# Kernel optimization log

Hardware: AMD Instinct MI355X
Metric: run time of the kernel (lower is better)

## Reference

```python
import jax, jax.numpy as jnp
import numpy as np

# Static graph layout: B equal-sized graphs of N nodes, DEG random edges per node.
B, N, DEG = 128, 1024, 16
F_IN, H, C = 2, 64, 2
RATIO = 0.8
E = B * N * DEG
K1 = int(np.ceil(RATIO * N))      # 820
K2 = int(np.ceil(RATIO * K1))     # 656
K3 = int(np.ceil(RATIO * K2))     # 525


def setup_inputs() -> dict:
    key = jax.random.key(0)
    ks = jax.random.split(key, 24)
    x = jax.random.normal(ks[0], (B * N, F_IN), jnp.float32)
    edge_attr = jax.random.uniform(ks[1], (E,), jnp.float32)
    # per-graph random endpoints, offset so edges stay inside each graph
    local = jax.random.randint(ks[2], (2, B, N * DEG), 0, N)
    edge_index = (local + (jnp.arange(B) * N)[None, :, None]).reshape(2, E)

    def lin(k, i, o):
        return jax.random.normal(k, (i, o), jnp.float32) / np.sqrt(i)

    def bias(k, o):
        return jax.random.normal(k, (o,), jnp.float32) * 0.01

    return {
        "x": x, "edge_attr": edge_attr,
        "W1": lin(ks[3], F_IN, H), "b1": bias(ks[4], H),
        "Wp1": lin(ks[5], H, 1), "bp1": bias(ks[6], 1),
        "W2": lin(ks[7], H, H), "b2": bias(ks[8], H),
        "Wp2": lin(ks[9], H, 1), "bp2": bias(ks[10], 1),
        "W3": lin(ks[11], H, H), "b3": bias(ks[12], H),
        "Wp3": lin(ks[13], H, 1), "bp3": bias(ks[14], 1),
        "Wl1": lin(ks[15], 2 * H, H), "bl1": bias(ks[16], H),
        "Wl2": lin(ks[17], H, H // 2), "bl2": bias(ks[18], H // 2),
        "Wl3": lin(ks[19], H // 2, C), "bl3": bias(ks[20], C),
        "edge_index": edge_index,
    }


def gcn(x, src, dst, w, W, b):
    """PyG GCNConv with gcn_norm (self-loops weight 1)."""
    h = x @ W                                       # [BN, out]
    deg = jnp.zeros((x.shape[0],), x.dtype).at[dst].add(w) + 1.0
    dinv = jax.lax.rsqrt(deg)
    norm = dinv[src] * w * dinv[dst]                # [E]
    out = jnp.zeros_like(h).at[dst].add(norm[:, None] * h[src])
    out = out + (dinv * dinv)[:, None] * h          # self-loop term
    return out + b


def sagpool(x, alive, src, dst, Wp, bp, k):
    """SAGPool: unweighted GCN scoring, per-graph top-k, x <- x * tanh(score).
    Removed nodes/edges are kept as masked (alive=False) slots -> static shapes."""
    we = (alive[src] & alive[dst]).astype(x.dtype)
    score = gcn(x, src, dst, we, Wp, bp)[:, 0]      # [BN]
    s = jnp.where(alive, score, -jnp.inf).reshape(B, N)
    _, idx = jax.lax.top_k(s, k)                    # [B, k]
    alive_new = jnp.zeros((B, N), bool).at[jnp.arange(B)[:, None], idx].set(True).reshape(-1)
    xn = jnp.where(alive_new[:, None], x * jnp.tanh(score)[:, None], 0.0)
    return xn, alive_new


def readout(x, alive):
    """concat(global_max_pool, global_mean_pool) over alive nodes per graph."""
    xr = x.reshape(B, N, -1)
    m = alive.reshape(B, N, 1)
    mx = jnp.max(jnp.where(m, xr, -jnp.inf), axis=1)
    mn = jnp.sum(jnp.where(m, xr, 0.0), axis=1) / jnp.sum(m, axis=1).astype(x.dtype)
    return jnp.concatenate([mx, mn], axis=1)        # [B, 2*H]


def _forward(x, edge_attr, W1, b1, Wp1, bp1, W2, b2, Wp2, bp2, W3, b3, Wp3, bp3,
             Wl1, bl1, Wl2, bl2, Wl3, bl3, edge_index):
    src, dst = edge_index[0], edge_index[1]
    h = jax.nn.relu(gcn(x, src, dst, edge_attr, W1, b1))
    h, a1 = sagpool(h, jnp.ones((B * N,), bool), src, dst, Wp1, bp1, K1)
    x1 = readout(h, a1)

    ea1 = edge_attr * (a1[src] & a1[dst]).astype(x.dtype)
    h = jax.nn.relu(gcn(h, src, dst, ea1, W2, b2))
    h, a2 = sagpool(h, a1, src, dst, Wp2, bp2, K2)
    x2 = readout(h, a2)

    # conv3 is called WITHOUT edge_weight -> surviving edges get weight 1
    ea2 = (a2[src] & a2[dst]).astype(x.dtype)
    h = jax.nn.relu(gcn(h, src, dst, ea2, W3, b3))
    h, a3 = sagpool(h, a2, src, dst, Wp3, bp3, K3)
    x3 = readout(h, a3)

    g = x1 + x2 + x3
    g = jax.nn.relu(g @ Wl1 + bl1)                  # dropout: eval mode (identity)
    g = jax.nn.relu(g @ Wl2 + bl2)
    return jax.nn.log_softmax(g @ Wl3 + bl3, axis=-1)


def reference(x, edge_attr, W1, b1, Wp1, bp1, W2, b2, Wp2, bp2, W3, b3, Wp3, bp3,
              Wl1, bl1, Wl2, bl2, Wl3, bl3, edge_index):
    return _forward(x, edge_attr, W1, b1, Wp1, bp1, W2, b2, Wp2, bp2, W3, b3,
                    Wp3, bp3, Wl1, bl1, Wl2, bl2, Wl3, bl3, edge_index)
```

## Files before the change

kernel.cpp:

```cpp
#include <hip/hip_runtime.h>
#include <math.h>

#define NB 128
#define NN 1024
#define BNODES (NB*NN)
#define NE 2097152
#define EPG (NE/NB)
#define EPT (EPG/NN)
#define FH 64
#define KK1 820
#define KK2 656
#define KK3 525

__global__ __launch_bounds__(1024) void k_csr(const int* __restrict__ ei,
                                              const float* __restrict__ ea,
                                              int* __restrict__ rowptr,
                                              int2* __restrict__ csr_sw,
                                              int* __restrict__ aliveA,
                                              float* __restrict__ dinvW,
                                              float* __restrict__ dinvU) {
  extern __shared__ int2 lcsr[];
  __shared__ int cnt[NN];
  __shared__ int cur[NN];
  __shared__ float wsum[NN];
  int b = blockIdx.x, t = threadIdx.x;
  int node = b*NN + t;
  aliveA[node] = 1;
  cnt[t] = 0;
  wsum[t] = 0.f;
  __syncthreads();
  int ebase = b*EPG;
  int se[EPT]; int de[EPT]; float we[EPT];
  #pragma unroll
  for (int i = 0; i < EPT; ++i) {
    int e = ebase + i*NN + t;
    se[i] = ei[e];
    de[i] = ei[NE + e] - b*NN;
    we[i] = ea[e];
    atomicAdd(&cnt[de[i]], 1);
    atomicAdd(&wsum[de[i]], we[i]);
  }
  __syncthreads();
  int v = cnt[t];
  for (int off = 1; off < NN; off <<= 1) {
    int u = (t >= off) ? cnt[t - off] : 0;
    __syncthreads();
    cnt[t] += u;
    __syncthreads();
  }
  int excl = cnt[t] - v;
  rowptr[node] = ebase + excl;
  cur[t] = excl;
  dinvW[node] = rsqrtf(1.f + wsum[t]);
  dinvU[node] = rsqrtf(1.f + (float)v);
  if (b == NB-1 && t == NN-1) rowptr[BNODES] = NE;
  __syncthreads();
  #pragma unroll
  for (int i = 0; i < EPT; ++i) {
    int pos = atomicAdd(&cur[de[i]], 1);
    lcsr[pos] = make_int2(se[i], __float_as_int(we[i]));
  }
  __syncthreads();
  float4* dst4 = (float4*)(csr_sw + ebase);
  const float4* src4 = (const float4*)lcsr;
  #pragma unroll
  for (int i = 0; i < EPG/2/NN; ++i)
    dst4[i*NN + t] = src4[i*NN + t];
}

template<int MODE>
__global__ void k_degs(const int* __restrict__ rowptr, const int2* __restrict__ csr_sw,
                       const int* __restrict__ alive,
                       float* __restrict__ dinvW, float* __restrict__ dinvU) {
  int t = threadIdx.x;
  int l16 = t & 15;
  int d = blockIdx.x*16 + (t >> 4);
  int r0 = rowptr[d], r1 = rowptr[d+1];
  float sW = 0.f, sU = 0.f;
  for (int base = r0; base < r1; base += 16) {
    if (base + l16 < r1) {
      int2 p = csr_sw[base + l16];
      if (alive[p.x]) { sW += (MODE == 2) ? 1.f : __int_as_float(p.y); sU += 1.f; }
    }
  }
  #pragma unroll
  for (int off = 8; off; off >>= 1) {
    sW += __shfl_xor(sW, off, 16);
    sU += __shfl_xor(sU, off, 16);
  }
  if (l16 == 0) {
    bool dA = (alive[d] != 0);
    dinvW[d] = dA ? rsqrtf(1.f + sW) : 0.f;
    dinvU[d] = dA ? rsqrtf(1.f + sU) : 0.f;
  }
}

__global__ void k_lin1(const float* __restrict__ x, const float* __restrict__ W,
                       float* __restrict__ h) {
  int i = blockIdx.x*256 + threadIdx.x;
  if (i >= BNODES*FH) return;
  int node = i >> 6, f = i & 63;
  h[i] = x[2*node]*W[f] + x[2*node+1]*W[FH + f];
}

__global__ void k_lin64(const float* __restrict__ hA, const float* __restrict__ tm,
                        const float* __restrict__ W, float* __restrict__ hB) {
  __shared__ float sX[64][65];
  __shared__ float sW[64*64];
  int t = threadIdx.x;
  for (int i = t; i < 1024; i += 256) ((float4*)sW)[i] = ((const float4*)W)[i];
  int nb = blockIdx.x * 64;
  #pragma unroll
  for (int i = 0; i < 16; ++i) {
    int gidx = (nb << 6) + i*256 + t;
    int node = gidx >> 6, f = gidx & 63;
    sX[node - nb][f] = hA[gidx] * tm[node];
  }
  __syncthreads();
  int node = t >> 2;
  int f0 = (t & 3) * 16;
  float4 a0 = {0,0,0,0}, a1 = a0, a2 = a0, a3 = a0;
  #pragma unroll 4
  for (int k = 0; k < 64; ++k) {
    float xv = sX[node][k];
    const float4 w0 = *(const float4*)&sW[k*64 + f0];
    const float4 w1 = *(const float4*)&sW[k*64 + f0 + 4];
    const float4 w2 = *(const float4*)&sW[k*64 + f0 + 8];
    const float4 w3 = *(const float4*)&sW[k*64 + f0 + 12];
    a0.x = fmaf(xv, w0.x, a0.x); a0.y = fmaf(xv, w0.y, a0.y);
    a0.z = fmaf(xv, w0.z, a0.z); a0.w = fmaf(xv, w0.w, a0.w);
    a1.x = fmaf(xv, w1.x, a1.x); a1.y = fmaf(xv, w1.y, a1.y);
    a1.z = fmaf(xv, w1.z, a1.z); a1.w = fmaf(xv, w1.w, a1.w);
    a2.x = fmaf(xv, w2.x, a2.x); a2.y = fmaf(xv, w2.y, a2.y);
    a2.z = fmaf(xv, w2.z, a2.z); a2.w = fmaf(xv, w2.w, a2.w);
    a3.x = fmaf(xv, w3.x, a3.x); a3.y = fmaf(xv, w3.y, a3.y);
    a3.z = fmaf(xv, w3.z, a3.z); a3.w = fmaf(xv, w3.w, a3.w);
  }
  float4* dst = (float4*)(hB + (size_t)(nb + node)*FH + f0);
  dst[0] = a0; dst[1] = a1; dst[2] = a2; dst[3] = a3;
}

template<int MODE>
__global__ void k_gather(const int* __restrict__ rowptr, const int2* __restrict__ csr_sw,
                         const float* __restrict__ dinvW, const float* __restrict__ dinvU,
                         const float* __restrict__ hB, const float* __restrict__ b,
                         const float* __restrict__ Wp,
                         float* __restrict__ hA, float* __restrict__ q) {
  int cpx = gridDim.x >> 3;
  int blk = (blockIdx.x & 7) * cpx + (blockIdx.x >> 3);
  int t = threadIdx.x;
  int l16 = t & 15;
  int d = blk*16 + (t >> 4);
  const float4* hB4 = (const float4*)hB;

  float dd = dinvW[d];
  float4 hv = hB4[(size_t)d*16 + l16];
  float4 bv = ((const float4*)b)[l16];
  float dd2 = dd*dd;
  float4 acc;
  acc.x = fmaf(dd2, hv.x, bv.x);
  acc.y = fmaf(dd2, hv.y, bv.y);
  acc.z = fmaf(dd2, hv.z, bv.z);
  acc.w = fmaf(dd2, hv.w, bv.w);

  int r0 = rowptr[d], r1 = rowptr[d+1];
  for (int base = r0; base < r1; base += 16) {
    int m = r1 - base;
    int sj = 0; float cj = 0.f;
    if (l16 < m) {
      int2 p = csr_sw[base + l16];
      sj = p.x;
      float w = (MODE == 2) ? 1.f : __int_as_float(p.y);
      cj = dinvW[sj] * w * dd;
    }
    #pragma unroll
    for (int j = 0; j < 16; ++j) {
      int s   = __shfl(sj, j, 16);
      float c = __shfl(cj, j, 16);
      float4 v = hB4[(size_t)s*16 + l16];
      acc.x = fmaf(c, v.x, acc.x);
      acc.y = fmaf(c, v.y, acc.y);
      acc.z = fmaf(c, v.z, acc.z);
      acc.w = fmaf(c, v.w, acc.w);
    }
  }
  acc.x = fmaxf(acc.x, 0.f); acc.y = fmaxf(acc.y, 0.f);
  acc.z = fmaxf(acc.z, 0.f); acc.w = fmaxf(acc.w, 0.f);
  ((float4*)hA)[(size_t)d*16 + l16] = acc;

  float4 wp = ((const float4*)Wp)[l16];
  float dot = acc.x*wp.x + acc.y*wp.y + acc.z*wp.z + acc.w*wp.w;
  #pragma unroll
  for (int off = 8; off; off >>= 1) dot += __shfl_xor(dot, off, 16);
  if (l16 == 0) q[d] = dinvU[d] * dot;
}

__global__ void k_score(const int* __restrict__ rowptr, const int2* __restrict__ csr_sw,
                        const float* __restrict__ dinvU, const float* __restrict__ q,
                        const float* __restrict__ bp, float* __restrict__ score) {
  int t = threadIdx.x;
  int l16 = t & 15;
  int d = blockIdx.x*16 + (t >> 4);
  float du = dinvU[d];
  float sum = 0.f;
  if (du != 0.f) {
    int r0 = rowptr[d], r1 = rowptr[d+1];
    for (int base = r0; base < r1; base += 16)
      if (base + l16 < r1) sum += q[csr_sw[base + l16].x];
  }
  #pragma unroll
  for (int off = 8; off; off >>= 1) sum += __shfl_xor(sum, off, 16);
  if (l16 == 0) score[d] = bp[0] + du*(q[d] + sum);
}

__global__ void k_topk(const float* __restrict__ score,
                       const int* __restrict__ alive, int k,
                       float* __restrict__ tm, int* __restrict__ aliveNext) {
  __shared__ float sc[NN];
  int b = blockIdx.x >> 2, p = blockIdx.x & 3;
  int t = threadIdx.x;
  int gbase = b*NN;
  #pragma unroll
  for (int i = 0; i < 4; ++i) {
    int n = i*256 + t;
    sc[n] = alive[gbase + n] ? score[gbase + n] : -INFINITY;
  }
  __syncthreads();
  int n = p*256 + t;
  int node = gbase + n;
  float me = sc[n];
  float raw = score[node];
  int rank = 0;
  const float4* sc4 = (const float4*)sc;
  for (int j4 = 0; j4 < NN/4; ++j4) {
    float4 o = sc4[j4];
    int jb = j4*4;
    rank += (o.x > me) || (o.x == me && jb+0 < n);
    rank += (o.y > me) || (o.y == me && jb+1 < n);
    rank += (o.z > me) || (o.z == me && jb+2 < n);
    rank += (o.w > me) || (o.w == me && jb+3 < n);
  }
  int sel = (rank < k) ? 1 : 0;
  aliveNext[node] = sel;
  tm[node] = sel ? tanhf(raw) : 0.f;
}

__global__ void k_sread(const float* __restrict__ hA, const float* __restrict__ tm,
                        const int* __restrict__ aliveN,
                        float* __restrict__ pmax, float* __restrict__ psum) {
  __shared__ float rm[4][FH], rs[4][FH];
  int b = blockIdx.x >> 2, p = blockIdx.x & 3;
  int t = threadIdx.x, f = t & 63, r = t >> 6;
  float mx = -INFINITY, sm = 0.f;
  for (int i = 0; i < 64; ++i) {
    int n = p*256 + i*4 + r;
    int node = b*NN + n;
    float v = hA[(size_t)node*FH + f] * tm[node];
    if (aliveN[node]) { mx = fmaxf(mx, v); sm += v; }
  }
  rm[r][f] = mx; rs[r][f] = sm;
  __syncthreads();
  if (t < FH) {
    float m2 = fmaxf(fmaxf(rm[0][t], rm[1][t]), fmaxf(rm[2][t], rm[3][t]));
    float s2 = rs[0][t] + rs[1][t] + rs[2][t] + rs[3][t];
    pmax[(b*4 + p)*FH + t] = m2;
    psum[(b*4 + p)*FH + t] = s2;
  }
}

__global__ void k_mlp(const float* __restrict__ pmax, const float* __restrict__ psum,
                      const float* __restrict__ Wl1, const float* __restrict__ bl1,
                      const float* __restrict__ Wl2, const float* __restrict__ bl2,
                      const float* __restrict__ Wl3, const float* __restrict__ bl3,
                      float* __restrict__ out) {
  __shared__ float sg[2*FH];
  __shared__ float l1[FH];
  __shared__ float l2[FH/2];
  __shared__ float l3[2];
  int b = blockIdx.x, t = threadIdx.x;
  const float kf[3] = {(float)KK1, (float)KK2, (float)KK3};
  float gm = 0.f, gs = 0.f;
  #pragma unroll
  for (int l = 0; l < 3; ++l) {
    const float* pm = pmax + (size_t)l*NB*4*FH + (b*4)*FH;
    const float* ps = psum + (size_t)l*NB*4*FH + (b*4)*FH;
    float mm = -INFINITY, ss = 0.f;
    #pragma unroll
    for (int p = 0; p < 4; ++p) {
      mm = fmaxf(mm, pm[p*FH + t]);
      ss += ps[p*FH + t];
    }
    gm += mm;
    gs += ss / kf[l];
  }
  sg[t] = gm;
  sg[FH + t] = gs;
  __syncthreads();
  float acc = bl1[t];
  #pragma unroll
  for (int k = 0; k < 2*FH; ++k) acc = fmaf(sg[k], Wl1[k*FH + t], acc);
  l1[t] = fmaxf(acc, 0.f);
  __syncthreads();
  if (t < 32) {
    float a2 = bl2[t];
    #pragma unroll
    for (int k = 0; k < FH; ++k) a2 = fmaf(l1[k], Wl2[k*32 + t], a2);
    l2[t] = fmaxf(a2, 0.f);
  }
  __syncthreads();
  if (t < 2) {
    float a3 = bl3[t];
    #pragma unroll
    for (int k = 0; k < 32; ++k) a3 = fmaf(l2[k], Wl3[k*2 + t], a3);
    l3[t] = a3;
  }
  __syncthreads();
  if (t == 0) {
    float m = fmaxf(l3[0], l3[1]);
    float lse = m + logf(expf(l3[0]-m) + expf(l3[1]-m));
    out[b*2+0] = l3[0] - lse;
    out[b*2+1] = l3[1] - lse;
  }
}

extern "C" void kernel_launch(void* const* d_in, const int* in_sizes, int n_in,
                              void* d_out, int out_size, void* d_ws, size_t ws_size,
                              hipStream_t stream) {
  const float* x   = (const float*)d_in[0];
  const float* ea  = (const float*)d_in[1];
  const float* W1  = (const float*)d_in[2];
  const float* b1  = (const float*)d_in[3];
  const float* Wp1 = (const float*)d_in[4];
  const float* bp1 = (const float*)d_in[5];
  const float* W2  = (const float*)d_in[6];
  const float* b2  = (const float*)d_in[7];
  const float* Wp2 = (const float*)d_in[8];
  const float* bp2 = (const float*)d_in[9];
  const float* W3  = (const float*)d_in[10];
  const float* b3  = (const float*)d_in[11];
  const float* Wp3 = (const float*)d_in[12];
  const float* bp3 = (const float*)d_in[13];
  const float* Wl1 = (const float*)d_in[14];
  const float* bl1 = (const float*)d_in[15];
  const float* Wl2 = (const float*)d_in[16];
  const float* bl2 = (const float*)d_in[17];
  const float* Wl3 = (const float*)d_in[18];
  const float* bl3 = (const float*)d_in[19];
  const int*   ei  = (const int*)d_in[20];
  float* out = (float*)d_out;

  int2* csr_sw = (int2*)d_ws;
  float* hA    = (float*)(csr_sw + NE);
  float* hB    = hA + (size_t)BNODES*FH;
  float* dinvW = hB + (size_t)BNODES*FH;
  float* dinvU = dinvW + BNODES;
  float* q     = dinvU + BNODES;
  float* score = q + BNODES;
  float* tm    = score + BNODES;
  float* pmax  = tm + BNODES;
  float* psum  = pmax + 3*NB*4*FH;
  int* aliveA  = (int*)(psum + 3*NB*4*FH);
  int* aliveB  = aliveA + BNODES;
  int* rowptr  = aliveB + BNODES;

  const int TB = 256;
  const int gG  = BNODES / 16;
  const int gNH = BNODES*FH / TB;
  const int gL  = BNODES / 64;

  k_csr<<<NB, 1024, EPG*sizeof(int2), stream>>>(ei, ea, rowptr, csr_sw, aliveA,
                                                dinvW, dinvU);

  k_lin1<<<gNH, TB, 0, stream>>>(x, W1, hB);
  k_gather<0><<<gG, TB, 0, stream>>>(rowptr, csr_sw, dinvW, dinvU, hB, b1, Wp1, hA, q);
  k_score<<<gG, TB, 0, stream>>>(rowptr, csr_sw, dinvU, q, bp1, score);
  k_topk<<<NB*4, TB, 0, stream>>>(score, aliveA, KK1, tm, aliveB);
  k_sread<<<NB*4, TB, 0, stream>>>(hA, tm, aliveB, pmax, psum);

  k_degs<1><<<gG, TB, 0, stream>>>(rowptr, csr_sw, aliveB, dinvW, dinvU);
  k_lin64<<<gL, TB, 0, stream>>>(hA, tm, W2, hB);
  k_gather<1><<<gG, TB, 0, stream>>>(rowptr, csr_sw, dinvW, dinvU, hB, b2, Wp2, hA, q);
  k_score<<<gG, TB, 0, stream>>>(rowptr, csr_sw, dinvU, q, bp2, score);
  k_topk<<<NB*4, TB, 0, stream>>>(score, aliveB, KK2, tm, aliveA);
  k_sread<<<NB*4, TB, 0, stream>>>(hA, tm, aliveA, pmax + NB*4*FH, psum + NB*4*FH);

  k_degs<2><<<gG, TB, 0, stream>>>(rowptr, csr_sw, aliveA, dinvW, dinvU);
  k_lin64<<<gL, TB, 0, stream>>>(hA, tm, W3, hB);
  k_gather<2><<<gG, TB, 0, stream>>>(rowptr, csr_sw, dinvW, dinvU, hB, b3, Wp3, hA, q);
  k_score<<<gG, TB, 0, stream>>>(rowptr, csr_sw, dinvU, q, bp3, score);
  k_topk<<<NB*4, TB, 0, stream>>>(score, aliveA, KK3, tm, aliveB);
  k_sread<<<NB*4, TB, 0, stream>>>(hA, tm, aliveB, pmax + 2*NB*4*FH, psum + 2*NB*4*FH);

  k_mlp<<<NB, FH, 0, stream>>>(pmax, psum, Wl1, bl1, Wl2, bl2, Wl3, bl3, out);
}
```

Baseline: 452.0 us.

## Stage per-graph feature halves in LDS for GCN neighbor gather

Replaces the per-node global-memory gather with a per-graph kernel: each block loads one graph's 1024 nodes times 32 features (half of the 64) plus the degree normalizers into shared memory, then aggregates neighbors from LDS. This relies on edges staying inside their graph. The score projection is split into two partial dot products, which a new small kernel combines and scales by dinvU. The point is to turn random global reads into LDS reads. In exchange the kernel uses 128KB of LDS per block, leaves only 256 blocks in flight, and adds an extra kernel launch per layer.

```diff
diff --git a/kernel.cpp b/kernel.cpp
--- a/kernel.cpp
+++ b/kernel.cpp
@@ -141,58 +141,78 @@
 }
 
 template<int MODE>
-__global__ void k_gather(const int* __restrict__ rowptr, const int2* __restrict__ csr_sw,
-                         const float* __restrict__ dinvW, const float* __restrict__ dinvU,
-                         const float* __restrict__ hB, const float* __restrict__ b,
-                         const float* __restrict__ Wp,
-                         float* __restrict__ hA, float* __restrict__ q) {
-  int cpx = gridDim.x >> 3;
-  int blk = (blockIdx.x & 7) * cpx + (blockIdx.x >> 3);
-  int t = threadIdx.x;
-  int l16 = t & 15;
-  int d = blk*16 + (t >> 4);
+__global__ __launch_bounds__(1024) void k_gath(
+    const int* __restrict__ rowptr, const int2* __restrict__ csr_sw,
+    const float* __restrict__ dinvW, const float* __restrict__ hB,
+    const float* __restrict__ bias, const float* __restrict__ Wp,
+    float* __restrict__ hA, float* __restrict__ qpart) {
+  extern __shared__ float sHB[];
+  __shared__ float sDW[NN];
+  __shared__ float sWp[32];
+  __shared__ float sB[32];
+  int b = blockIdx.x >> 1, half = blockIdx.x & 1;
+  int t = threadIdx.x, l8 = t & 7;
+  int gbase = b*NN;
+  sDW[t] = dinvW[gbase + t];
+  if (t < 32) { sWp[t] = Wp[half*32 + t]; sB[t] = bias[half*32 + t]; }
   const float4* hB4 = (const float4*)hB;
-
-  float dd = dinvW[d];
-  float4 hv = hB4[(size_t)d*16 + l16];
-  float4 bv = ((const float4*)b)[l16];
-  float dd2 = dd*dd;
-  float4 acc;
-  acc.x = fmaf(dd2, hv.x, bv.x);
-  acc.y = fmaf(dd2, hv.y, bv.y);
-  acc.z = fmaf(dd2, hv.z, bv.z);
-  acc.w = fmaf(dd2, hv.w, bv.w);
-
-  int r0 = rowptr[d], r1 = rowptr[d+1];
-  for (int base = r0; base < r1; base += 16) {
-    int m = r1 - base;
-    int sj = 0; float cj = 0.f;
-    if (l16 < m) {
-      int2 p = csr_sw[base + l16];
-      sj = p.x;
-      float w = (MODE == 2) ? 1.f : __int_as_float(p.y);
-      cj = dinvW[sj] * w * dd;
+  float4* sHB4 = (float4*)sHB;
+  #pragma unroll
+  for (int i = 0; i < 8; ++i) {
+    int idx = i*1024 + t;
+    int n = idx >> 3, j = idx & 7;
+    sHB4[n*8 + j] = hB4[(size_t)(gbase + n)*16 + half*8 + j];
+  }
+  __syncthreads();
+  float4 bv = ((const float4*)sB)[l8];
+  float4 wp = ((const float4*)sWp)[l8];
+  #pragma unroll 1
+  for (int pass = 0; pass < 8; ++pass) {
+    int n = pass*128 + (t >> 3);
+    int gn = gbase + n;
+    float dd = sDW[n];
+    float4 hv = sHB4[n*8 + l8];
+    float dd2 = dd*dd;
+    float4 acc;
+    acc.x = fmaf(dd2, hv.x, bv.x);
+    acc.y = fmaf(dd2, hv.y, bv.y);
+    acc.z = fmaf(dd2, hv.z, bv.z);
+    acc.w = fmaf(dd2, hv.w, bv.w);
+    int r0 = rowptr[gn], r1 = rowptr[gn+1];
+    for (int base = r0; base < r1; base += 8) {
+      int sj = 0; float cj = 0.f;
+      if (base + l8 < r1) {
+        int2 p = csr_sw[base + l8];
+        sj = p.x - gbase;
+        float w = (MODE == 2) ? 1.f : __int_as_float(p.y);
+        cj = sDW[sj] * w * dd;
+      }
+      #pragma unroll
+      for (int j = 0; j < 8; ++j) {
+        int s   = __shfl(sj, j, 8);
+        float c = __shfl(cj, j, 8);
+        float4 v = sHB4[s*8 + l8];
+        acc.x = fmaf(c, v.x, acc.x);
+        acc.y = fmaf(c, v.y, acc.y);
+        acc.z = fmaf(c, v.z, acc.z);
+        acc.w = fmaf(c, v.w, acc.w);
+      }
     }
-    #pragma unroll
-    for (int j = 0; j < 16; ++j) {
-      int s   = __shfl(sj, j, 16);
-      float c = __shfl(cj, j, 16);
-      float4 v = hB4[(size_t)s*16 + l16];
-      acc.x = fmaf(c, v.x, acc.x);
-      acc.y = fmaf(c, v.y, acc.y);
-      acc.z = fmaf(c, v.z, acc.z);
-      acc.w = fmaf(c, v.w, acc.w);
-    }
-  }
-  acc.x = fmaxf(acc.x, 0.f); acc.y = fmaxf(acc.y, 0.f);
-  acc.z = fmaxf(acc.z, 0.f); acc.w = fmaxf(acc.w, 0.f);
-  ((float4*)hA)[(size_t)d*16 + l16] = acc;
-
-  float4 wp = ((const float4*)Wp)[l16];
-  float dot = acc.x*wp.x + acc.y*wp.y + acc.z*wp.z + acc.w*wp.w;
-  #pragma unroll
-  for (int off = 8; off; off >>= 1) dot += __shfl_xor(dot, off, 16);
-  if (l16 == 0) q[d] = dinvU[d] * dot;
+    acc.x = fmaxf(acc.x, 0.f); acc.y = fmaxf(acc.y, 0.f);
+    acc.z = fmaxf(acc.z, 0.f); acc.w = fmaxf(acc.w, 0.f);
+    ((float4*)hA)[(size_t)gn*16 + half*8 + l8] = acc;
+    float dot = acc.x*wp.x + acc.y*wp.y + acc.z*wp.z + acc.w*wp.w;
+    dot += __shfl_xor(dot, 4, 8);
+    dot += __shfl_xor(dot, 2, 8);
+    dot += __shfl_xor(dot, 1, 8);
+    if (l8 == 0) qpart[half*BNODES + gn] = dot;
+  }
+}
+
+__global__ void k_qfin(const float* __restrict__ dinvU, const float* __restrict__ qp,
+                       float* __restrict__ q) {
+  int i = blockIdx.x*256 + threadIdx.x;
+  if (i < BNODES) q[i] = dinvU[i]*(qp[i] + qp[BNODES + i]);
 }
 
 __global__ void k_score(const int* __restrict__ rowptr, const int2* __restrict__ csr_sw,
@@ -355,7 +375,8 @@
   float* dinvW = hB + (size_t)BNODES*FH;
   float* dinvU = dinvW + BNODES;
   float* q     = dinvU + BNODES;
-  float* score = q + BNODES;
+  float* qpart = q + BNODES;
+  float* score = qpart + 2*BNODES;
   float* tm    = score + BNODES;
   float* pmax  = tm + BNODES;
   float* psum  = pmax + 3*NB*4*FH;
@@ -367,26 +388,31 @@
   const int gG  = BNODES / 16;
   const int gNH = BNODES*FH / TB;
   const int gL  = BNODES / 64;
+  const int gN  = BNODES / TB;
+  const size_t gathLds = (size_t)NN*32*sizeof(float);
 
   k_csr<<<NB, 1024, EPG*sizeof(int2), stream>>>(ei, ea, rowptr, csr_sw, aliveA,
                                                 dinvW, dinvU);
 
   k_lin1<<<gNH, TB, 0, stream>>>(x, W1, hB);
-  k_gather<0><<<gG, TB, 0, stream>>>(rowptr, csr_sw, dinvW, dinvU, hB, b1, Wp1, hA, q);
+  k_gath<0><<<NB*2, 1024, gathLds, stream>>>(rowptr, csr_sw, dinvW, hB, b1, Wp1, hA, qpart);
+  k_qfin<<<gN, TB, 0, stream>>>(dinvU, qpart, q);
   k_score<<<gG, TB, 0, stream>>>(rowptr, csr_sw, dinvU, q, bp1, score);
   k_topk<<<NB*4, TB, 0, stream>>>(score, aliveA, KK1, tm, aliveB);
   k_sread<<<NB*4, TB, 0, stream>>>(hA, tm, aliveB, pmax, psum);
 
   k_degs<1><<<gG, TB, 0, stream>>>(rowptr, csr_sw, aliveB, dinvW, dinvU);
   k_lin64<<<gL, TB, 0, stream>>>(hA, tm, W2, hB);
-  k_gather<1><<<gG, TB, 0, stream>>>(rowptr, csr_sw, dinvW, dinvU, hB, b2, Wp2, hA, q);
+  k_gath<1><<<NB*2, 1024, gathLds, stream>>>(rowptr, csr_sw, dinvW, hB, b2, Wp2, hA, qpart);
+  k_qfin<<<gN, TB, 0, stream>>>(dinvU, qpart, q);
   k_score<<<gG, TB, 0, stream>>>(rowptr, csr_sw, dinvU, q, bp2, score);
   k_topk<<<NB*4, TB, 0, stream>>>(score, aliveB, KK2, tm, aliveA);
   k_sread<<<NB*4, TB, 0, stream>>>(hA, tm, aliveA, pmax + NB*4*FH, psum + NB*4*FH);
 
   k_degs<2><<<gG, TB, 0, stream>>>(rowptr, csr_sw, aliveA, dinvW, dinvU);
   k_lin64<<<gL, TB, 0, stream>>>(hA, tm, W3, hB);
-  k_gather<2><<<gG, TB, 0, stream>>>(rowptr, csr_sw, dinvW, dinvU, hB, b3, Wp3, hA, q);
+  k_gath<2><<<NB*2, 1024, gathLds, stream>>>(rowptr, csr_sw, dinvW, hB, b3, Wp3, hA, qpart);
+  k_qfin<<<gN, TB, 0, stream>>>(dinvU, qpart, q);
   k_score<<<gG, TB, 0, stream>>>(rowptr, csr_sw, dinvU, q, bp3, score);
   k_topk<<<NB*4, TB, 0, stream>>>(score, aliveA, KK3, tm, aliveB);
   k_sread<<<NB*4, TB, 0, stream>>>(hA, tm, aliveB, pmax + 2*NB*4*FH, psum + 2*NB*4*FH);
```

New measurement: 452.0 us. About the same (-0.0%).
